# Kernel optimization log

Hardware: AMD Instinct MI355X
Metric: run time of the kernel (lower is better)

Reference implementation:

```python
import jax, jax.numpy as jnp
import numpy as np

N_NODES = 100000
N_EDGES = 1600000
D_FEAT = 64


def setup_inputs() -> dict:
    key = jax.random.key(0)
    k1, k2, k3 = jax.random.split(key, 3)
    embeddings = jax.random.normal(k1, (N_NODES, D_FEAT), dtype=jnp.float32)
    src = jax.random.randint(k2, (N_EDGES,), 0, N_NODES)
    dst = jax.random.randint(k3, (N_EDGES,), 0, N_NODES)
    return {"embeddings": embeddings, "src": src, "dst": dst, "n_nodes": N_NODES}


def reference(embeddings, src, dst, n_nodes):
    # SmoothFilter with norm='both': D^{-1/2} A D^{-1/2} X  (GCN propagation)
    ones = jnp.ones(src.shape[0], dtype=embeddings.dtype)
    out_deg = jnp.clip(jax.ops.segment_sum(ones, src, num_segments=n_nodes), 1.0)
    in_deg = jnp.clip(jax.ops.segment_sum(ones, dst, num_segments=n_nodes), 1.0)
    # pre-normalize by out-degree^{-1/2}
    h = embeddings * (out_deg ** -0.5)[:, None]          # [N, d]
    # copy_src + sum aggregation over edges (sparse neighbor sum)
    agg = jax.ops.segment_sum(h[src], dst, num_segments=n_nodes)  # [N, d]
    # post-normalize by in-degree^{-1/2}
    return agg * (in_deg ** -0.5)[:, None]
```

## Files before the change

kernel.cpp:

```cpp
#include <hip/hip_runtime.h>
#include <hip/hip_fp16.h>

#define D_FEAT 64
#define NPB 128
#define NBMAX 1024
#define SBSH 9
#define SNPB 512
#define SBMAX 256
#define CHUNK 4096
#define EPT 16
#define CAPB 2816
#define CAPB_H 1536
#define RPT 6

__global__ void zero_ints(int* __restrict__ p, int n) {
    int i = blockIdx.x * blockDim.x + threadIdx.x;
    int stride = gridDim.x * blockDim.x;
    for (int j = i; j < n; j += stride) p[j] = 0;
}

__global__ __launch_bounds__(256) void bcnt_kernel(
        const int* __restrict__ src, const int* __restrict__ dst, int n_edges,
        int* __restrict__ dbcnt8, int* __restrict__ sbcnt8) {
    __shared__ int ld[NBMAX];
    __shared__ int ls[SBMAX];
    int t = threadIdx.x;
    for (int i = t; i < NBMAX; i += 256) ld[i] = 0;
    if (t < SBMAX) ls[t] = 0;
    __syncthreads();
    int i0 = blockIdx.x * blockDim.x + t;
    int stride = gridDim.x * blockDim.x;
    for (int e = i0; e < n_edges; e += stride) {
        atomicAdd(&ld[dst[e] >> 7], 1);
        atomicAdd(&ls[src[e] >> SBSH], 1);
    }
    __syncthreads();
    int* dmy = dbcnt8 + (blockIdx.x & 7) * NBMAX;
    int* smy = sbcnt8 + (blockIdx.x & 7) * SBMAX;
    for (int i = t; i < NBMAX; i += 256) {
        if (ld[i]) atomicAdd(&dmy[i], ld[i]);
    }
    if (t < SBMAX && ls[t]) atomicAdd(&smy[t], ls[t]);
}

__global__ void scan2_kernel(const int* __restrict__ dbcnt8, const int* __restrict__ sbcnt8,
                             int* __restrict__ dbstart, int* __restrict__ gcursor,
                             int* __restrict__ sbstart, int* __restrict__ scursor,
                             int n_edges) {
    __shared__ int wsum[16];
    int t = threadIdx.x, lane = t & 63, w = t >> 6;
    if (blockIdx.x == 0) {
        int v = 0;
        #pragma unroll
        for (int c = 0; c < 8; ++c) v += dbcnt8[c * NBMAX + t];
        int inc = v;
        #pragma unroll
        for (int off = 1; off < 64; off <<= 1) {
            int y = __shfl_up(inc, off);
            if (lane >= off) inc += y;
        }
        if (lane == 63) wsum[w] = inc;
        __syncthreads();
        int add = 0;
        #pragma unroll
        for (int i = 0; i < 15; ++i) if (i < w) add += wsum[i];
        int ex = add + inc - v;
        dbstart[t] = ex;
        gcursor[t] = ex;
        if (t == NBMAX - 1) dbstart[NBMAX] = n_edges;
    } else {
        int v = 0, inc = 0;
        if (t < SBMAX) {
            #pragma unroll
            for (int c = 0; c < 8; ++c) v += sbcnt8[c * SBMAX + t];
            inc = v;
            #pragma unroll
            for (int off = 1; off < 64; off <<= 1) {
                int y = __shfl_up(inc, off);
                if (lane >= off) inc += y;
            }
            if (lane == 63) wsum[w] = inc;
        }
        __syncthreads();
        if (t < SBMAX) {
            int add = 0;
            #pragma unroll
            for (int i = 0; i < 3; ++i) if (i < w) add += wsum[i];
            int ex = add + inc - v;
            sbstart[t] = ex;
            scursor[t] = ex;
            if (t == SBMAX - 1) sbstart[SBMAX] = n_edges;
        }
    }
}

__global__ __launch_bounds__(256) void dualpart_kernel(
        const int* __restrict__ src, const int* __restrict__ dst, int n_edges,
        int* __restrict__ gcursor, int* __restrict__ scursor,
        int* __restrict__ arrA, unsigned short* __restrict__ arrS16) {
    __shared__ int lhist[NBMAX];
    __shared__ int lstart[NBMAX];
    __shared__ int ldelta[NBMAX];
    __shared__ int lcur[NBMAX];
    __shared__ int part[256];
    __shared__ int pkLDS[CHUNK];
    __shared__ unsigned short bktLDS[CHUNK];

    int t = threadIdx.x;
    long long cbase = (long long)blockIdx.x * CHUNK;
    int cnt = (n_edges - cbase < CHUNK) ? (int)(n_edges - cbase) : CHUNK;

    for (int i = t; i < NBMAX; i += 256) lhist[i] = 0;
    __syncthreads();

    int ssrc[EPT], sdst[EPT];
    #pragma unroll
    for (int i = 0; i < EPT; ++i) {
        long long e = cbase + t + i * 256;
        if (e < n_edges) {
            ssrc[i] = src[e];
            sdst[i] = dst[e];
            atomicAdd(&lhist[sdst[i] >> 7], 1);
        } else {
            ssrc[i] = -1;
            sdst[i] = -1;
        }
    }
    __syncthreads();

    int b0 = 4 * t;
    int h0 = lhist[b0], h1 = lhist[b0 + 1], h2v = lhist[b0 + 2], h3 = lhist[b0 + 3];
    int tot = h0 + h1 + h2v + h3;
    part[t] = tot;
    __syncthreads();
    for (int off = 1; off < 256; off <<= 1) {
        int x = (t >= off) ? part[t - off] : 0;
        __syncthreads();
        part[t] += x;
        __syncthreads();
    }
    int ex = part[t] - tot;
    lstart[b0] = ex;
    lstart[b0 + 1] = ex + h0;
    lstart[b0 + 2] = ex + h0 + h1;
    lstart[b0 + 3] = ex + h0 + h1 + h2v;
    __syncthreads();
    for (int b = t; b < NBMAX; b += 256) {
        lcur[b] = lstart[b];
        int c = lhist[b];
        if (c > 0) ldelta[b] = atomicAdd(&gcursor[b], c) - lstart[b];
    }
    __syncthreads();
    #pragma unroll
    for (int i = 0; i < EPT; ++i) {
        if (sdst[i] >= 0) {
            int b = sdst[i] >> 7;
            int slot = atomicAdd(&lcur[b], 1);
            pkLDS[slot] = (ssrc[i] << 7) | (sdst[i] & 127);
            bktLDS[slot] = (unsigned short)b;
        }
    }
    __syncthreads();
    for (int j = t; j < cnt; j += 256) {
        int b = bktLDS[j];
        arrA[j + ldelta[b]] = pkLDS[j];
    }
    __syncthreads();

    if (t < SBMAX) lhist[t] = 0;
    __syncthreads();
    #pragma unroll
    for (int i = 0; i < EPT; ++i) {
        if (ssrc[i] >= 0) atomicAdd(&lhist[ssrc[i] >> SBSH], 1);
    }
    __syncthreads();
    int h = lhist[t];
    part[t] = h;
    __syncthreads();
    for (int off = 1; off < 256; off <<= 1) {
        int x = (t >= off) ? part[t - off] : 0;
        __syncthreads();
        part[t] += x;
        __syncthreads();
    }
    ex = part[t] - h;
    lcur[t] = ex;
    if (h > 0) ldelta[t] = atomicAdd(&scursor[t], h) - ex;
    __syncthreads();
    unsigned short* stg = (unsigned short*)pkLDS;
    #pragma unroll
    for (int i = 0; i < EPT; ++i) {
        if (ssrc[i] >= 0) {
            int b = ssrc[i] >> SBSH;
            int slot = atomicAdd(&lcur[b], 1);
            stg[slot] = (unsigned short)(ssrc[i] & (SNPB - 1));
            bktLDS[slot] = (unsigned short)b;
        }
    }
    __syncthreads();
    for (int j = t; j < cnt; j += 256) {
        int b = bktLDS[j];
        arrS16[j + ldelta[b]] = stg[j];
    }
}

__global__ __launch_bounds__(256) void prep_kernel(
        const float4* __restrict__ emb4, const unsigned short* __restrict__ arrS16,
        const int* __restrict__ sbstart, uint2* __restrict__ h2, int n_nodes) {
    __shared__ int lh[SNPB];
    __shared__ float lsc[SNPB];
    int b = blockIdx.x, t = threadIdx.x;
    int s = sbstart[b], e = sbstart[b + 1];
    for (int i = t; i < SNPB; i += 256) lh[i] = 0;
    __syncthreads();
    for (int i = s + t; i < e; i += 256) atomicAdd(&lh[arrS16[i]], 1);
    __syncthreads();
    for (int i = t; i < SNPB; i += 256) {
        int od = lh[i];
        lsc[i] = rsqrtf((float)(od > 1 ? od : 1));
    }
    __syncthreads();
    int nbase = b * SNPB;
    int r = t >> 4, c = t & 15;
    for (int r0 = 0; r0 < SNPB; r0 += 16) {
        int row = r0 + r;
        int node = nbase + row;
        if (node < n_nodes) {
            float sc = lsc[row];
            float4 v = emb4[(size_t)node * 16 + c];
            __half2 a = __floats2half2_rn(v.x * sc, v.y * sc);
            __half2 bb = __floats2half2_rn(v.z * sc, v.w * sc);
            union { __half2 h; unsigned int u; } ua, ub;
            ua.h = a; ub.h = bb;
            uint2 rr; rr.x = ua.u; rr.y = ub.u;
            h2[(size_t)node * 16 + c] = rr;
        }
    }
    if (b == 0 && t < 16) {
        uint2 z; z.x = 0; z.y = 0;
        h2[(size_t)n_nodes * 16 + t] = z;
    }
}

__global__ __launch_bounds__(512) void sortagg_kernel(
        const uint2* __restrict__ h2, const int* __restrict__ arrA,
        const int* __restrict__ dbstart, float* __restrict__ out, int n_nodes) {
    __shared__ int lh[64];
    __shared__ int lst[64];
    __shared__ int lcur[64];
    __shared__ int srcS[CAPB_H];
    int b = blockIdx.x >> 1, half = blockIdx.x & 1;
    int t = threadIdx.x;
    int s = dbstart[b], e = dbstart[b + 1];
    int cnt = e - s;
    bool fit = (cnt <= CAPB);

    if (t < 64) lh[t] = 0;
    __syncthreads();
    int pkreg[RPT];
    if (fit) {
        #pragma unroll
        for (int i = 0; i < RPT; ++i) {
            int idx = t + i * 512;
            int pk = (idx < cnt) ? arrA[s + idx] : -1;
            pkreg[i] = pk;
            if (pk >= 0 && (((pk >> 6) & 1) == half)) atomicAdd(&lh[pk & 63], 1);
        }
    } else {
        for (int i = t; i < cnt; i += 512) {
            int v = arrA[s + i];
            if (((v >> 6) & 1) == half) atomicAdd(&lh[v & 63], 1);
        }
    }
    __syncthreads();
    if (t < 64) {
        int l0 = lh[t];
        int a = l0;
        #pragma unroll
        for (int off = 1; off < 64; off <<= 1) {
            int y = __shfl_up(a, off);
            if (t >= off) a += y;
        }
        lst[t] = a - l0;
        lcur[t] = a - l0;
    }
    __syncthreads();
    int halfcnt = lst[63] + lh[63];
    bool useS = fit && (halfcnt <= CAPB_H);
    if (useS) {
        #pragma unroll
        for (int i = 0; i < RPT; ++i) {
            int pk = pkreg[i];
            if (pk >= 0 && (((pk >> 6) & 1) == half)) {
                int slot = atomicAdd(&lcur[pk & 63], 1);
                srcS[slot] = pk >> 7;
            }
        }
    }
    __syncthreads();

    int w = t >> 6, L = t & 63, g = L >> 4, c = L & 15;
    int nbase = b * NPB + half * 64;
    union { unsigned int u; __half2 h; } uc;
    for (int nl = w * 8; nl < w * 8 + 8; ++nl) {
        int node = nbase + nl;
        if (node >= n_nodes) break;
        int st = lst[nl];
        int deg = lh[nl];
        int en = st + deg;
        float ax = 0.f, ay = 0.f, az = 0.f, aw = 0.f;
        if (useS) {
            for (int eidx = st; eidx < en; eidx += 16) {
                int ea = eidx + g, eb = ea + 4, ec = ea + 8, ed = ea + 12;
                int sa = (ea < en) ? srcS[ea] : n_nodes;
                int sb = (eb < en) ? srcS[eb] : n_nodes;
                int sc = (ec < en) ? srcS[ec] : n_nodes;
                int sd = (ed < en) ? srcS[ed] : n_nodes;
                uint2 va = h2[(size_t)sa * 16 + c];
                uint2 vb = h2[(size_t)sb * 16 + c];
                uint2 vc = h2[(size_t)sc * 16 + c];
                uint2 vd = h2[(size_t)sd * 16 + c];
                float2 f;
                uc.u = va.x; f = __half22float2(uc.h); ax += f.x; ay += f.y;
                uc.u = va.y; f = __half22float2(uc.h); az += f.x; aw += f.y;
                uc.u = vb.x; f = __half22float2(uc.h); ax += f.x; ay += f.y;
                uc.u = vb.y; f = __half22float2(uc.h); az += f.x; aw += f.y;
                uc.u = vc.x; f = __half22float2(uc.h); ax += f.x; ay += f.y;
                uc.u = vc.y; f = __half22float2(uc.h); az += f.x; aw += f.y;
                uc.u = vd.x; f = __half22float2(uc.h); ax += f.x; ay += f.y;
                uc.u = vd.y; f = __half22float2(uc.h); az += f.x; aw += f.y;
            }
        } else {
            int hv = (half << 6) | nl;
            for (int i2 = g; i2 < cnt; i2 += 4) {
                int v = arrA[s + i2];
                if ((v & 127) == hv) {
                    int sa = v >> 7;
                    uint2 va = h2[(size_t)sa * 16 + c];
                    float2 f;
                    uc.u = va.x; f = __half22float2(uc.h); ax += f.x; ay += f.y;
                    uc.u = va.y; f = __half22float2(uc.h); az += f.x; aw += f.y;
                }
            }
        }
        ax += __shfl_xor(ax, 16); ay += __shfl_xor(ay, 16);
        az += __shfl_xor(az, 16); aw += __shfl_xor(aw, 16);
        ax += __shfl_xor(ax, 32); ay += __shfl_xor(ay, 32);
        az += __shfl_xor(az, 32); aw += __shfl_xor(aw, 32);
        if (g == 0) {
            float is = rsqrtf((float)(deg > 1 ? deg : 1));
            float4 r;
            r.x = ax * is; r.y = ay * is; r.z = az * is; r.w = aw * is;
            ((float4*)out)[(size_t)node * 16 + c] = r;
        }
    }
}

__global__ void fb_zero(float* __restrict__ out, long long n_out,
                        int* __restrict__ deg, int n_deg) {
    long long i = (long long)blockIdx.x * blockDim.x + threadIdx.x;
    long long stride = (long long)gridDim.x * blockDim.x;
    for (long long j = i; j < n_out; j += stride) out[j] = 0.0f;
    for (long long j = i; j < n_deg; j += stride) deg[j] = 0;
}

__global__ void fb_degree(const int* __restrict__ src, const int* __restrict__ dst,
                          int n_edges, int* __restrict__ outdeg, int* __restrict__ indeg) {
    int i = blockIdx.x * blockDim.x + threadIdx.x;
    int stride = gridDim.x * blockDim.x;
    for (int e = i; e < n_edges; e += stride) {
        atomicAdd(&outdeg[src[e]], 1);
        atomicAdd(&indeg[dst[e]], 1);
    }
}

__global__ void fb_scatter(const float* __restrict__ emb,
                           const int* __restrict__ src, const int* __restrict__ dst,
                           const int* __restrict__ outdeg,
                           float* __restrict__ out, int n_edges) {
    const int epb = blockDim.x >> 6;
    const int d = threadIdx.x & 63;
    long long e0 = (long long)blockIdx.x * epb + (threadIdx.x >> 6);
    long long estride = (long long)gridDim.x * epb;
    for (long long e = e0; e < n_edges; e += estride) {
        int s = src[e];
        int tt = dst[e];
        int od = outdeg[s];
        float v = emb[(long long)s * D_FEAT + d] * rsqrtf((float)(od > 1 ? od : 1));
        atomicAdd(&out[(long long)tt * D_FEAT + d], v);
    }
}

__global__ void fb_scale(float* __restrict__ out, const int* __restrict__ indeg,
                         long long n_elems) {
    long long i = (long long)blockIdx.x * blockDim.x + threadIdx.x;
    long long stride = (long long)gridDim.x * blockDim.x;
    for (long long j = i; j < n_elems; j += stride) {
        int id = indeg[(int)(j >> 6)];
        out[j] *= rsqrtf((float)(id > 1 ? id : 1));
    }
}

extern "C" void kernel_launch(void* const* d_in, const int* in_sizes, int n_in,
                              void* d_out, int out_size, void* d_ws, size_t ws_size,
                              hipStream_t stream) {
    const float* emb = (const float*)d_in[0];
    const int* src = (const int*)d_in[1];
    const int* dst = (const int*)d_in[2];
    const int n_nodes = in_sizes[0] / D_FEAT;
    const int n_edges = in_sizes[1];
    float* out = (float*)d_out;
    const int block = 256;
    const int nb = (n_nodes + NPB - 1) / NPB;
    const int nb2 = (n_nodes + SNPB - 1) / SNPB;
    const int K = NBMAX;

    int* dbcnt8 = (int*)d_ws;
    int* sbcnt8 = dbcnt8 + 8 * K;
    int* dbstart = sbcnt8 + 8 * SBMAX;
    int* gcursor = dbstart + K + 1;
    int* sbstart = gcursor + K;
    int* scursor = sbstart + SBMAX + 1;
    int* arrA = scursor + SBMAX;
    int* region = arrA + n_edges;
    unsigned short* arrS16 = (unsigned short*)region;
    uint2* h2 = (uint2*)region;

    size_t region_ints = (size_t)(n_nodes + 1) * 32;
    size_t arrS_ints = ((size_t)n_edges + 1) / 2;
    if (arrS_ints > region_ints) region_ints = arrS_ints;
    size_t need = (8 * (size_t)K + 8 * SBMAX + (K + 1) + K + (SBMAX + 1) + SBMAX
                   + (size_t)n_edges + region_ints) * sizeof(int);

    if (ws_size >= need && nb <= K && nb2 <= SBMAX) {
        zero_ints<<<32, block, 0, stream>>>(dbcnt8, 8 * K + 8 * SBMAX);
        bcnt_kernel<<<384, block, 0, stream>>>(src, dst, n_edges, dbcnt8, sbcnt8);
        scan2_kernel<<<2, K, 0, stream>>>(dbcnt8, sbcnt8, dbstart, gcursor,
                                          sbstart, scursor, n_edges);
        int pblocks = (n_edges + CHUNK - 1) / CHUNK;
        dualpart_kernel<<<pblocks, 256, 0, stream>>>(src, dst, n_edges, gcursor,
                                                     scursor, arrA, arrS16);
        prep_kernel<<<nb2, 256, 0, stream>>>((const float4*)emb, arrS16, sbstart,
                                             h2, n_nodes);
        sortagg_kernel<<<2 * nb, 512, 0, stream>>>(h2, arrA, dbstart, out, n_nodes);
    } else {
        int* foutdeg = (int*)d_ws;
        int* findeg = foutdeg + n_nodes;
        long long n_out = (long long)n_nodes * D_FEAT;
        fb_zero<<<2048, block, 0, stream>>>(out, n_out, foutdeg, 2 * n_nodes);
        fb_degree<<<2048, block, 0, stream>>>(src, dst, n_edges, foutdeg, findeg);
        fb_scatter<<<2048, block, 0, stream>>>(emb, src, dst, foutdeg, out, n_edges);
        fb_scale<<<2048, block, 0, stream>>>(out, findeg, n_out);
    }
}
```

Baseline: 127.2 us.

## Split degree-scale computation from fp16 prepass and shrink aggregation blocks to 256

The fused prep kernel is split in two. One kernel counts out-degrees per super-bucket and writes a per-node float scale to workspace. A separate grid-stride kernel converts the embeddings to fp16 and zero-pads the sentinel row. The aggregation kernel moves from 512 to 256 threads per block, so each wave now handles 16 nodes. It also drops the register caching of packed edge entries and reads arrA from global twice instead. The aim is better occupancy and more parallelism in the fp16 conversion, at the cost of an extra launch, an extra scale array, and repeated edge reads.

```diff
diff --git a/kernel.cpp b/kernel.cpp
--- a/kernel.cpp
+++ b/kernel.cpp
@@ -11,7 +11,6 @@
 #define EPT 16
 #define CAPB 2816
 #define CAPB_H 1536
-#define RPT 6
 
 __global__ void zero_ints(int* __restrict__ p, int n) {
     int i = blockIdx.x * blockDim.x + threadIdx.x;
@@ -204,45 +203,50 @@
     }
 }
 
-__global__ __launch_bounds__(256) void prep_kernel(
-        const float4* __restrict__ emb4, const unsigned short* __restrict__ arrS16,
-        const int* __restrict__ sbstart, uint2* __restrict__ h2, int n_nodes) {
+__global__ __launch_bounds__(256) void scount_kernel(
+        const unsigned short* __restrict__ arrS16, const int* __restrict__ sbstart,
+        float* __restrict__ oscale, int n_nodes) {
     __shared__ int lh[SNPB];
-    __shared__ float lsc[SNPB];
     int b = blockIdx.x, t = threadIdx.x;
     int s = sbstart[b], e = sbstart[b + 1];
     for (int i = t; i < SNPB; i += 256) lh[i] = 0;
     __syncthreads();
     for (int i = s + t; i < e; i += 256) atomicAdd(&lh[arrS16[i]], 1);
     __syncthreads();
+    int nbase = b * SNPB;
     for (int i = t; i < SNPB; i += 256) {
-        int od = lh[i];
-        lsc[i] = rsqrtf((float)(od > 1 ? od : 1));
-    }
-    __syncthreads();
-    int nbase = b * SNPB;
-    int r = t >> 4, c = t & 15;
-    for (int r0 = 0; r0 < SNPB; r0 += 16) {
-        int row = r0 + r;
-        int node = nbase + row;
+        int node = nbase + i;
         if (node < n_nodes) {
-            float sc = lsc[row];
-            float4 v = emb4[(size_t)node * 16 + c];
-            __half2 a = __floats2half2_rn(v.x * sc, v.y * sc);
-            __half2 bb = __floats2half2_rn(v.z * sc, v.w * sc);
+            int od = lh[i];
+            oscale[node] = rsqrtf((float)(od > 1 ? od : 1));
+        }
+    }
+}
+
+__global__ void h_prepass_kernel(const float4* __restrict__ emb4,
+                                 const float* __restrict__ oscale,
+                                 uint2* __restrict__ h2, int n_total, int n_nodes) {
+    int i = blockIdx.x * blockDim.x + threadIdx.x;
+    int stride = gridDim.x * blockDim.x;
+    for (int j = i; j < n_total; j += stride) {
+        int node = j >> 4;
+        uint2 r;
+        if (node < n_nodes) {
+            float s = oscale[node];
+            float4 v = emb4[j];
+            __half2 a = __floats2half2_rn(v.x * s, v.y * s);
+            __half2 b = __floats2half2_rn(v.z * s, v.w * s);
             union { __half2 h; unsigned int u; } ua, ub;
-            ua.h = a; ub.h = bb;
-            uint2 rr; rr.x = ua.u; rr.y = ub.u;
-            h2[(size_t)node * 16 + c] = rr;
-        }
-    }
-    if (b == 0 && t < 16) {
-        uint2 z; z.x = 0; z.y = 0;
-        h2[(size_t)n_nodes * 16 + t] = z;
-    }
-}
-
-__global__ __launch_bounds__(512) void sortagg_kernel(
+            ua.h = a; ub.h = b;
+            r.x = ua.u; r.y = ub.u;
+        } else {
+            r.x = 0; r.y = 0;
+        }
+        h2[j] = r;
+    }
+}
+
+__global__ __launch_bounds__(256) void sortagg_kernel(
         const uint2* __restrict__ h2, const int* __restrict__ arrA,
         const int* __restrict__ dbstart, float* __restrict__ out, int n_nodes) {
     __shared__ int lh[64];
@@ -253,24 +257,12 @@
     int t = threadIdx.x;
     int s = dbstart[b], e = dbstart[b + 1];
     int cnt = e - s;
-    bool fit = (cnt <= CAPB);
 
     if (t < 64) lh[t] = 0;
     __syncthreads();
-    int pkreg[RPT];
-    if (fit) {
-        #pragma unroll
-        for (int i = 0; i < RPT; ++i) {
-            int idx = t + i * 512;
-            int pk = (idx < cnt) ? arrA[s + idx] : -1;
-            pkreg[i] = pk;
-            if (pk >= 0 && (((pk >> 6) & 1) == half)) atomicAdd(&lh[pk & 63], 1);
-        }
-    } else {
-        for (int i = t; i < cnt; i += 512) {
-            int v = arrA[s + i];
-            if (((v >> 6) & 1) == half) atomicAdd(&lh[v & 63], 1);
-        }
+    for (int i = t; i < cnt; i += 256) {
+        int v = arrA[s + i];
+        if (((v >> 6) & 1) == half) atomicAdd(&lh[v & 63], 1);
     }
     __syncthreads();
     if (t < 64) {
@@ -286,14 +278,13 @@
     }
     __syncthreads();
     int halfcnt = lst[63] + lh[63];
-    bool useS = fit && (halfcnt <= CAPB_H);
+    bool useS = (halfcnt <= CAPB_H);
     if (useS) {
-        #pragma unroll
-        for (int i = 0; i < RPT; ++i) {
-            int pk = pkreg[i];
-            if (pk >= 0 && (((pk >> 6) & 1) == half)) {
-                int slot = atomicAdd(&lcur[pk & 63], 1);
-                srcS[slot] = pk >> 7;
+        for (int i = t; i < cnt; i += 256) {
+            int v = arrA[s + i];
+            if (((v >> 6) & 1) == half) {
+                int slot = atomicAdd(&lcur[v & 63], 1);
+                srcS[slot] = v >> 7;
             }
         }
     }
@@ -302,7 +293,7 @@
     int w = t >> 6, L = t & 63, g = L >> 4, c = L & 15;
     int nbase = b * NPB + half * 64;
     union { unsigned int u; __half2 h; } uc;
-    for (int nl = w * 8; nl < w * 8 + 8; ++nl) {
+    for (int nl = w * 16; nl < w * 16 + 16; ++nl) {
         int node = nbase + nl;
         if (node >= n_nodes) break;
         int st = lst[nl];
@@ -415,7 +406,8 @@
     const int nb2 = (n_nodes + SNPB - 1) / SNPB;
     const int K = NBMAX;
 
-    int* dbcnt8 = (int*)d_ws;
+    float* oscale = (float*)d_ws;
+    int* dbcnt8 = (int*)(oscale + n_nodes);
     int* sbcnt8 = dbcnt8 + 8 * K;
     int* dbstart = sbcnt8 + 8 * SBMAX;
     int* gcursor = dbstart + K + 1;
@@ -429,8 +421,8 @@
     size_t region_ints = (size_t)(n_nodes + 1) * 32;
     size_t arrS_ints = ((size_t)n_edges + 1) / 2;
     if (arrS_ints > region_ints) region_ints = arrS_ints;
-    size_t need = (8 * (size_t)K + 8 * SBMAX + (K + 1) + K + (SBMAX + 1) + SBMAX
-                   + (size_t)n_edges + region_ints) * sizeof(int);
+    size_t need = ((size_t)n_nodes + 8 * (size_t)K + 8 * SBMAX + (K + 1) + K
+                   + (SBMAX + 1) + SBMAX + (size_t)n_edges + region_ints) * sizeof(int);
 
     if (ws_size >= need && nb <= K && nb2 <= SBMAX) {
         zero_ints<<<32, block, 0, stream>>>(dbcnt8, 8 * K + 8 * SBMAX);
@@ -440,9 +432,11 @@
         int pblocks = (n_edges + CHUNK - 1) / CHUNK;
         dualpart_kernel<<<pblocks, 256, 0, stream>>>(src, dst, n_edges, gcursor,
                                                      scursor, arrA, arrS16);
-        prep_kernel<<<nb2, 256, 0, stream>>>((const float4*)emb, arrS16, sbstart,
-                                             h2, n_nodes);
-        sortagg_kernel<<<2 * nb, 512, 0, stream>>>(h2, arrA, dbstart, out, n_nodes);
+        scount_kernel<<<nb2, 256, 0, stream>>>(arrS16, sbstart, oscale, n_nodes);
+        int n_total = (n_nodes + 1) * 16;
+        h_prepass_kernel<<<2048, block, 0, stream>>>((const float4*)emb, oscale,
+                                                     h2, n_total, n_nodes);
+        sortagg_kernel<<<2 * nb, 256, 0, stream>>>(h2, arrA, dbstart, out, n_nodes);
     } else {
         int* foutdeg = (int*)d_ws;
         int* findeg = foutdeg + n_nodes;
```

Result: slower. 130.6 us (+2.7%).
